# Kernel optimization log

Measured on AMD Instinct MI355X. Metric: run time of the kernel, lower is better.

Reference implementation:

```python
import jax, jax.numpy as jnp
import numpy as np

N, E, IN, H, C = 50000, 1600000, 256, 256, 2


def _lin(k, o, i):
    return (jax.random.normal(k, (o, i), jnp.float32) / np.sqrt(i)).astype(jnp.float32)


def setup_inputs() -> dict:
    key = jax.random.key(0)
    ks = jax.random.split(key, 16)
    x = jax.random.normal(ks[0], (N, IN), jnp.float32)
    edge_index = jax.random.randint(ks[1], (2, E), 0, N, dtype=jnp.int32)
    return dict(
        x=x, edge_index=edge_index,
        W1=_lin(ks[2], H, IN), b1=0.01 * jax.random.normal(ks[10], (H,), jnp.float32),
        W2=_lin(ks[3], H, H), b2=0.01 * jax.random.normal(ks[11], (H,), jnp.float32),
        W3=_lin(ks[4], H, H), b3=0.01 * jax.random.normal(ks[12], (H,), jnp.float32),
        W4=_lin(ks[5], C, H), b4=0.01 * jax.random.normal(ks[13], (C,), jnp.float32),
        T10=_lin(ks[6], H, H), T11=_lin(ks[7], H, H), cb1=0.01 * jax.random.normal(ks[14], (H,), jnp.float32),
        T20=_lin(ks[8], H, H), T21=_lin(ks[9], H, H), cb2=0.01 * jax.random.normal(ks[15], (H,), jnp.float32),
    )


def _cheb_norm(edge_index, n):
    # PyG ChebConv, normalization='sym', lambda_max=2.0:
    # L_hat = 2/lambda_max * (I - D^-1/2 A D^-1/2) - I = -D^-1/2 A D^-1/2
    # (the +I and -I self-loop terms cancel), so only off-diagonal norm remains.
    row, col = edge_index[0], edge_index[1]
    deg = jax.ops.segment_sum(jnp.ones((edge_index.shape[1],), jnp.float32), row, num_segments=n)
    dis = jnp.where(deg > 0, jax.lax.rsqrt(jnp.where(deg > 0, deg, 1.0)), 0.0)
    return -dis[row] * dis[col]  # [E]


def _cheb_conv(x, edge_index, norm, W0, W1, b, n):
    # K=2: out = Tx_0 @ W0^T + Tx_1 @ W1^T + b, Tx_0 = x, Tx_1 = L_hat x
    src, dst = edge_index[0], edge_index[1]  # message: x_j from src, aggregate at dst
    tx1 = jax.ops.segment_sum(norm[:, None] * x[src], dst, num_segments=n)
    return x @ W0.T + tx1 @ W1.T + b


def reference(x, edge_index, W1, b1, W2, b2, W3, b3, W4, b4, T10, T11, cb1, T20, T21, cb2):
    n = x.shape[0]
    norm = _cheb_norm(edge_index, n)
    h = jax.nn.relu(x @ W1.T + b1)
    h = jax.nn.relu(h @ W2.T + b2)
    h = _cheb_conv(h, edge_index, norm, T10, T11, cb1, n)
    h = _cheb_conv(h, edge_index, norm, T20, T21, cb2, n)
    h = jax.nn.relu(h @ W3.T + b3)
    return h @ W4.T + b4
```

## Files before the change

### kernel.cpp

```cpp
#include <hip/hip_runtime.h>

#define HDIM 256
#define NHB 256
#define NBINB 50048
#define NBINW (NBINB/4)
#define NBAND 16

typedef __attribute__((ext_vector_type(8))) short short8v;
typedef __attribute__((ext_vector_type(4))) short short4v;
typedef __attribute__((ext_vector_type(4))) float floatx4;

static __device__ __forceinline__ unsigned short f2bf(float f) {
    union { float f; unsigned u; } c; c.f = f;
    unsigned u = c.u;
    unsigned r = u + 0x7FFFu + ((u >> 16) & 1u);
    return (unsigned short)(r >> 16);
}
static __device__ __forceinline__ float bf2f(unsigned short h) {
    union { unsigned u; float f; } c; c.u = ((unsigned)h) << 16;
    return c.f;
}


__global__ __launch_bounds__(512) void hist_k(const int* __restrict__ src, const int* __restrict__ dst,
                                              unsigned int* __restrict__ degS, unsigned int* __restrict__ cntS,
                                              int nE) {
    __shared__ unsigned int h8[NBINW];
    const int tid = threadIdx.x;
    const int isDst = blockIdx.x >= NHB;
    const int bb = isDst ? blockIdx.x - NHB : blockIdx.x;
    const int* __restrict__ arr = isDst ? dst : src;
    unsigned int* __restrict__ outS = isDst ? cntS : degS;

    for (int i = tid; i < NBINW; i += 512) h8[i] = 0u;
    __syncthreads();
    const int chunk = (nE + NHB - 1) / NHB;
    const int e0 = bb * chunk;
    const int e1 = min(e0 + chunk, nE);
    for (int e = e0 + tid; e < e1; e += 512) {
        int n = arr[e];
        atomicAdd(&h8[n >> 2], 1u << ((n & 3) << 3));
    }
    __syncthreads();
    unsigned int* __restrict__ row = outS + (size_t)bb * NBINW;
    for (int i = tid; i < NBINW; i += 512) row[i] = h8[i];
}


__global__ __launch_bounds__(256) void reduce_k(const unsigned char* __restrict__ degS,
                                                unsigned char* __restrict__ cntS,
                                                float* __restrict__ dis, int* __restrict__ tmp,
                                                int* __restrict__ bsums, int nN) {
    __shared__ int s[256];
    const int t = threadIdx.x;
    const int n = blockIdx.x * 256 + t;
    int run = 0;
    if (n < nN) {
        int d = 0;
        #pragma unroll 8
        for (int b = 0; b < NHB; ++b) d += degS[(size_t)b * NBINB + n];
        dis[n] = (d > 0) ? (1.0f / sqrtf((float)d)) : 0.0f;
        unsigned r = 0;
        #pragma unroll 4
        for (int b = 0; b < NHB; ++b) {
            size_t o = (size_t)b * NBINB + n;
            unsigned c = cntS[o];
            cntS[o] = (unsigned char)r;
            r += c;
        }
        run = (int)r;
    }
    s[t] = run; __syncthreads();
    #pragma unroll
    for (int off = 1; off < 256; off <<= 1) {
        int x = (t >= off) ? s[t - off] : 0;
        __syncthreads();
        s[t] += x;
        __syncthreads();
    }
    if (n < nN) tmp[n] = s[t];
    if (t == 255) bsums[blockIdx.x] = s[255];
}


__global__ __launch_bounds__(256) void scan3_k(const int* __restrict__ tmp, const int* __restrict__ bsums,
                                               int* __restrict__ offs, int nN, int nE, int nb) {
    __shared__ int s[256];
    const int t = threadIdx.x;
    int v = (t < nb) ? bsums[t] : 0;
    s[t] = v; __syncthreads();
    #pragma unroll
    for (int off = 1; off < 256; off <<= 1) {
        int x = (t >= off) ? s[t - off] : 0;
        __syncthreads();
        s[t] += x;
        __syncthreads();
    }
    const int base = (blockIdx.x > 0) ? s[blockIdx.x - 1] : 0;
    __syncthreads();
    const int i = blockIdx.x * 256 + t;
    if (i < nN) {
        int prev = (t > 0) ? tmp[i - 1] : 0;
        offs[i] = base + prev;
    }
    if (i == nN - 1) offs[nN] = nE;
}


__global__ __launch_bounds__(512) void fill_k(const int* __restrict__ src, const int* __restrict__ dst,
                                              const float* __restrict__ dis, const int* __restrict__ offs,
                                              const unsigned int* __restrict__ cntS,
                                              int2* __restrict__ csr, int nE) {
    __shared__ unsigned int cur8[NBINW];
    const int tid = threadIdx.x;
    const int bb = blockIdx.x;
    const unsigned int* __restrict__ baseRow = cntS + (size_t)bb * NBINW;
    for (int i = tid; i < NBINW; i += 512) cur8[i] = baseRow[i];
    __syncthreads();
    const int chunk = (nE + NHB - 1) / NHB;
    const int e0 = bb * chunk;
    const int e1 = min(e0 + chunk, nE);
    for (int e = e0 + tid; e < e1; e += 512) {
        int s = src[e], d = dst[e];
        unsigned sh = (unsigned)(d & 3) << 3;
        unsigned old = atomicAdd(&cur8[d >> 2], 1u << sh);
        unsigned c = (old >> sh) & 0xFFu;
        int p = offs[d] + (int)c;
        float w = -dis[s] * dis[d];
        csr[p] = make_int2(s, __float_as_int(w));
    }
}


struct WPtrs { const float* w[7]; };
__global__ __launch_bounds__(256) void wsplit_all_k(WPtrs ws, unsigned short* __restrict__ base) {
    int wi = blockIdx.x >> 6;
    int idx = (blockIdx.x & 63) * 256 + threadIdx.x;
    const float* w = ws.w[wi];
    unsigned short* hi = base + (size_t)wi * 131072;
    unsigned short* lo = hi + 65536;
    float4 v = ((const float4*)w)[idx];
    float f[4] = {v.x, v.y, v.z, v.w};
    short4v hv, lv;
    #pragma unroll
    for (int e = 0; e < 4; ++e) {
        unsigned short h = f2bf(f[e]);
        float rem = f[e] - bf2f(h);
        hv[e] = (short)h;
        lv[e] = (short)f2bf(rem);
    }
    *(short4v*)(hi + idx * 4) = hv;
    *(short4v*)(lo + idx * 4) = lv;
}


#define LDP 40

__global__ __launch_bounds__(512, 4) void mfma_gemm_k(
    const float* __restrict__ AF,
    const unsigned short* __restrict__ Ah0, const unsigned short* __restrict__ Al0,
    const unsigned short* __restrict__ Wh0, const unsigned short* __restrict__ Wl0,
    const unsigned short* __restrict__ Ah1, const unsigned short* __restrict__ Al1,
    const unsigned short* __restrict__ Wh1, const unsigned short* __restrict__ Wl1,
    const float* __restrict__ bias,
    float* __restrict__ outF, unsigned short* __restrict__ outHi, unsigned short* __restrict__ outLo,
    const float* __restrict__ W4f, const float* __restrict__ b4f, float* __restrict__ outFinal,
    int nRows, int relu, int dual)
{
    __shared__ short Ahs[128 * LDP];
    __shared__ short Als[128 * LDP];
    __shared__ short Bhs[256 * LDP];
    __shared__ short Bls[256 * LDP];

    const int tid  = threadIdx.x;
    const int lane = tid & 63;
    const int wv   = tid >> 6;
    const int wm   = wv >> 2, wn = wv & 3;
    const int lrow = lane & 15, kg = lane >> 4;
    const int row0 = blockIdx.x * 128;

    const int sr = tid >> 2, sc = tid & 3;
    int agr = row0 + sr; if (agr >= nRows) agr = nRows - 1;

    floatx4 acc[4][4];
    #pragma unroll
    for (int i = 0; i < 4; ++i)
        #pragma unroll
        for (int j = 0; j < 4; ++j)
            acc[i][j] = (floatx4)0.0f;

    const int npass = dual ? 2 : 1;
    for (int pass = 0; pass < npass; ++pass) {
        const unsigned short* __restrict__ Ah = pass ? Ah1 : Ah0;
        const unsigned short* __restrict__ Al = pass ? Al1 : Al0;
        const unsigned short* __restrict__ Wh = pass ? Wh1 : Wh0;
        const unsigned short* __restrict__ Wl = pass ? Wl1 : Wl0;
        const bool f32A = (pass == 0) && (AF != nullptr);
        for (int k0 = 0; k0 < HDIM; k0 += 32) {
            __syncthreads();
            if (f32A) {
                const float* pa = AF + (size_t)agr * HDIM + k0 + sc * 8;
                float4 v0 = *(const float4*)pa;
                float4 v1 = *(const float4*)(pa + 4);
                float f[8] = {v0.x, v0.y, v0.z, v0.w, v1.x, v1.y, v1.z, v1.w};
                short8v hv, lv;
                #pragma unroll
                for (int e = 0; e < 8; ++e) {
                    unsigned short h = f2bf(f[e]);
                    float rem = f[e] - bf2f(h);
                    hv[e] = (short)h;
                    lv[e] = (short)f2bf(rem);
                }
                *(short8v*)(Ahs + sr * LDP + sc * 8) = hv;
                *(short8v*)(Als + sr * LDP + sc * 8) = lv;
            } else {
                size_t ga = (size_t)agr * HDIM + k0 + sc * 8;
                *(short8v*)(Ahs + sr * LDP + sc * 8) = *(const short8v*)(Ah + ga);
                *(short8v*)(Als + sr * LDP + sc * 8) = *(const short8v*)(Al + ga);
            }
            #pragma unroll
            for (int q = 0; q < 2; ++q) {
                int idx = tid + q * 512;
                int br = idx >> 2, bc = idx & 3;
                size_t gb = (size_t)br * HDIM + k0 + bc * 8;
                *(short8v*)(Bhs + br * LDP + bc * 8) = *(const short8v*)(Wh + gb);
                *(short8v*)(Bls + br * LDP + bc * 8) = *(const short8v*)(Wl + gb);
            }
            __syncthreads();

            short8v ahf[4], alf[4];
            #pragma unroll
            for (int fm = 0; fm < 4; ++fm) {
                int ra = (wm * 64 + fm * 16 + lrow) * LDP + kg * 8;
                ahf[fm] = *(const short8v*)(Ahs + ra);
                alf[fm] = *(const short8v*)(Als + ra);
            }
            #pragma unroll
            for (int fn = 0; fn < 4; ++fn) {
                int rb = (wn * 64 + fn * 16 + lrow) * LDP + kg * 8;
                short8v bh = *(const short8v*)(Bhs + rb);
                short8v bl = *(const short8v*)(Bls + rb);
                #pragma unroll
                for (int fm = 0; fm < 4; ++fm) {
                    acc[fm][fn] = __builtin_amdgcn_mfma_f32_16x16x32_bf16(ahf[fm], bh, acc[fm][fn], 0, 0, 0);
                    acc[fm][fn] = __builtin_amdgcn_mfma_f32_16x16x32_bf16(ahf[fm], bl, acc[fm][fn], 0, 0, 0);
                    acc[fm][fn] = __builtin_amdgcn_mfma_f32_16x16x32_bf16(alf[fm], bh, acc[fm][fn], 0, 0, 0);
                }
            }
        }
    }

    if (outFinal) {
        float w40[4], w41[4];
        #pragma unroll
        for (int fn = 0; fn < 4; ++fn) {
            int col = wn * 64 + fn * 16 + lrow;
            w40[fn] = W4f[col];
            w41[fn] = W4f[HDIM + col];
        }
        float p0[4][4], p1[4][4];
        #pragma unroll
        for (int fm = 0; fm < 4; ++fm)
            #pragma unroll
            for (int r = 0; r < 4; ++r) { p0[fm][r] = 0.f; p1[fm][r] = 0.f; }
        #pragma unroll
        for (int fn = 0; fn < 4; ++fn) {
            int col = wn * 64 + fn * 16 + lrow;
            float bv = bias[col];
            #pragma unroll
            for (int fm = 0; fm < 4; ++fm)
                #pragma unroll
                for (int r = 0; r < 4; ++r) {
                    float v = fmaxf(acc[fm][fn][r] + bv, 0.0f);
                    p0[fm][r] = fmaf(v, w40[fn], p0[fm][r]);
                    p1[fm][r] = fmaf(v, w41[fn], p1[fm][r]);
                }
        }
        #pragma unroll
        for (int fm = 0; fm < 4; ++fm)
            #pragma unroll
            for (int r = 0; r < 4; ++r) {
                #pragma unroll
                for (int m = 1; m < 16; m <<= 1) {
                    p0[fm][r] += __shfl_xor(p0[fm][r], m, 64);
                    p1[fm][r] += __shfl_xor(p1[fm][r], m, 64);
                }
            }
        __syncthreads();
        float* red = (float*)Ahs;
        if (lrow == 0) {
            #pragma unroll
            for (int fm = 0; fm < 4; ++fm)
                #pragma unroll
                for (int r = 0; r < 4; ++r) {
                    int rl = wm * 64 + fm * 16 + kg * 4 + r;
                    red[(wn * 128 + rl) * 2 + 0] = p0[fm][r];
                    red[(wn * 128 + rl) * 2 + 1] = p1[fm][r];
                }
        }
        __syncthreads();
        if (tid < 256) {
            int rl = tid >> 1, j = tid & 1;
            int grow = row0 + rl;
            if (grow < nRows) {
                float s = b4f[j]
                        + red[(0 * 128 + rl) * 2 + j] + red[(1 * 128 + rl) * 2 + j]
                        + red[(2 * 128 + rl) * 2 + j] + red[(3 * 128 + rl) * 2 + j];
                outFinal[(size_t)grow * 2 + j] = s;
            }
        }
        return;
    }

    #pragma unroll
    for (int fn = 0; fn < 4; ++fn) {
        int col = wn * 64 + fn * 16 + lrow;
        float bv = bias[col];
        #pragma unroll
        for (int fm = 0; fm < 4; ++fm) {
            #pragma unroll
            for (int r = 0; r < 4; ++r) {
                int grow = row0 + wm * 64 + fm * 16 + kg * 4 + r;
                if (grow < nRows) {
                    float v = acc[fm][fn][r] + bv;
                    if (relu) v = fmaxf(v, 0.0f);
                    size_t o = (size_t)grow * HDIM + col;
                    if (outF) outF[o] = v;
                    if (outHi) {
                        unsigned short h = f2bf(v);
                        outHi[o] = h;
                        outLo[o] = f2bf(v - bf2f(h));
                    }
                }
            }
        }
    }
}


#define ACC4(m0, m1, m2, m3)                                                    \
    {                                                                           \
        const uint2 g0 = *(const uint2*)(hb + (size_t)m0.x * HDIM + lane * 4);  \
        const uint2 g1 = *(const uint2*)(hb + (size_t)m1.x * HDIM + lane * 4);  \
        const uint2 g2 = *(const uint2*)(hb + (size_t)m2.x * HDIM + lane * 4);  \
        const uint2 g3 = *(const uint2*)(hb + (size_t)m3.x * HDIM + lane * 4);  \
        float w0 = __int_as_float(m0.y), w1 = __int_as_float(m1.y);             \
        float w2 = __int_as_float(m2.y), w3 = __int_as_float(m3.y);             \
        a0 = fmaf(w0, __uint_as_float(g0.x << 16), a0);                         \
        a1 = fmaf(w0, __uint_as_float(g0.x & 0xffff0000u), a1);                 \
        a2 = fmaf(w0, __uint_as_float(g0.y << 16), a2);                         \
        a3 = fmaf(w0, __uint_as_float(g0.y & 0xffff0000u), a3);                 \
        a0 = fmaf(w1, __uint_as_float(g1.x << 16), a0);                         \
        a1 = fmaf(w1, __uint_as_float(g1.x & 0xffff0000u), a1);                 \
        a2 = fmaf(w1, __uint_as_float(g1.y << 16), a2);                         \
        a3 = fmaf(w1, __uint_as_float(g1.y & 0xffff0000u), a3);                 \
        a0 = fmaf(w2, __uint_as_float(g2.x << 16), a0);                         \
        a1 = fmaf(w2, __uint_as_float(g2.x & 0xffff0000u), a1);                 \
        a2 = fmaf(w2, __uint_as_float(g2.y << 16), a2);                         \
        a3 = fmaf(w2, __uint_as_float(g2.y & 0xffff0000u), a3);                 \
        a0 = fmaf(w3, __uint_as_float(g3.x << 16), a0);                         \
        a1 = fmaf(w3, __uint_as_float(g3.x & 0xffff0000u), a1);                 \
        a2 = fmaf(w3, __uint_as_float(g3.y << 16), a2);                         \
        a3 = fmaf(w3, __uint_as_float(g3.y & 0xffff0000u), a3);                 \
    }

#define ACC1(m)                                                                 \
    {                                                                           \
        const uint2 g = *(const uint2*)(hb + (size_t)m.x * HDIM + lane * 4);    \
        float wt = __int_as_float(m.y);                                         \
        a0 = fmaf(wt, __uint_as_float(g.x << 16), a0);                          \
        a1 = fmaf(wt, __uint_as_float(g.x & 0xffff0000u), a1);                  \
        a2 = fmaf(wt, __uint_as_float(g.y << 16), a2);                          \
        a3 = fmaf(wt, __uint_as_float(g.y & 0xffff0000u), a3);                  \
    }

__global__ __launch_bounds__(256) void aggregate_k(
    const unsigned short* __restrict__ hb, const int2* __restrict__ csr,
    const int* __restrict__ offs,
    unsigned short* __restrict__ outHi, unsigned short* __restrict__ outLo)
{
    __shared__ float red[4][256];
    __shared__ int2 sorted[256];
    __shared__ unsigned bins[NBAND];
    __shared__ unsigned cur[NBAND];

    const int n = blockIdx.x;
    const int tid = threadIdx.x;
    const int w = tid >> 6;
    const int lane = tid & 63;
    const int start = offs[n], end = offs[n + 1];
    const int deg = end - start;

    float a0 = 0.f, a1 = 0.f, a2 = 0.f, a3 = 0.f;

    if (deg <= 256) {
        if (tid < NBAND) { bins[tid] = 0u; }
        __syncthreads();
        int2 my; int myband = 0;
        if (tid < deg) {
            my = csr[start + tid];
            myband = my.x >> 12;
            atomicAdd(&bins[myband], 1u);
        }
        __syncthreads();
        if (tid == 0) {
            unsigned run = 0;
            #pragma unroll
            for (int b = 0; b < NBAND; ++b) { unsigned c = bins[b]; cur[b] = run; run += c; }
        }
        __syncthreads();
        if (tid < deg) {
            unsigned pos = atomicAdd(&cur[myband], 1u);
            sorted[pos] = my;
        }
        __syncthreads();

        int e = w;
        for (; e + 12 < deg; e += 16) {
            int2 m0 = sorted[e], m1 = sorted[e + 4], m2 = sorted[e + 8], m3 = sorted[e + 12];
            ACC4(m0, m1, m2, m3);
        }
        for (; e < deg; e += 4) {
            int2 m = sorted[e];
            ACC1(m);
        }
    } else {
        int e = start + w;
        for (; e + 12 < end; e += 16) {
            int2 m0 = csr[e], m1 = csr[e + 4], m2 = csr[e + 8], m3 = csr[e + 12];
            ACC4(m0, m1, m2, m3);
        }
        for (; e < end; e += 4) {
            int2 m = csr[e];
            ACC1(m);
        }
    }

    red[w][lane * 4 + 0] = a0;
    red[w][lane * 4 + 1] = a1;
    red[w][lane * 4 + 2] = a2;
    red[w][lane * 4 + 3] = a3;
    __syncthreads();

    const int t = threadIdx.x;
    float s = red[0][t] + red[1][t] + red[2][t] + red[3][t];
    size_t o = (size_t)n * HDIM + t;
    unsigned short h = f2bf(s);
    outHi[o] = h;
    outLo[o] = f2bf(s - bf2f(h));
}


extern "C" void kernel_launch(void* const* d_in, const int* in_sizes, int n_in,
                              void* d_out, int out_size, void* d_ws, size_t ws_size,
                              hipStream_t stream) {
    const float* x   = (const float*)d_in[0];
    const int*   ei  = (const int*)d_in[1];
    const float* W1  = (const float*)d_in[2];
    const float* b1  = (const float*)d_in[3];
    const float* W2  = (const float*)d_in[4];
    const float* b2  = (const float*)d_in[5];
    const float* W3  = (const float*)d_in[6];
    const float* b3  = (const float*)d_in[7];
    const float* W4  = (const float*)d_in[8];
    const float* b4  = (const float*)d_in[9];
    const float* T10 = (const float*)d_in[10];
    const float* T11 = (const float*)d_in[11];
    const float* cb1 = (const float*)d_in[12];
    const float* T20 = (const float*)d_in[13];
    const float* T21 = (const float*)d_in[14];
    const float* cb2 = (const float*)d_in[15];

    const int nN = in_sizes[0] / HDIM;
    const int nE = in_sizes[1] / 2;
    const int* src = ei;
    const int* dst = ei + nE;

    char* p = (char*)d_ws;
    auto alloc = [&](size_t bytes) { void* r = (void*)p; p += (bytes + 255) & ~(size_t)255; return r; };
    float* dis     = (float*)alloc((size_t)nN * 4);
    int*   tmp     = (int*)alloc((size_t)nN * 4);
    int*   bsums   = (int*)alloc(1024 * 4);
    int*   offs    = (int*)alloc((size_t)(nN + 1) * 4);
    int2*  csr     = (int2*)alloc((size_t)nE * 8);
    unsigned int* degS = (unsigned int*)alloc((size_t)NHB * NBINB);
    unsigned int* cntS = (unsigned int*)alloc((size_t)NHB * NBINB);
    const size_t NH = (size_t)nN * HDIM;
    unsigned short* Xh  = (unsigned short*)alloc(NH * 4);  unsigned short* Xl  = Xh + NH;
    unsigned short* Ahp = (unsigned short*)alloc(NH * 4);  unsigned short* Alp = Ahp + NH;
    unsigned short* Bhp = (unsigned short*)alloc(NH * 4);  unsigned short* Blp = Bhp + NH;
    unsigned short* Dhp = (unsigned short*)alloc(NH * 4);  unsigned short* Dlp = Dhp + NH;
    unsigned short* wsp = (unsigned short*)alloc((size_t)7 * 131072 * 2);

    float* out = (float*)d_out;
    const int nbN = (nN + 255) / 256;

    hist_k<<<2 * NHB, 512, 0, stream>>>(src, dst, degS, cntS, nE);
    reduce_k<<<nbN, 256, 0, stream>>>((const unsigned char*)degS, (unsigned char*)cntS,
                                      dis, tmp, bsums, nN);
    scan3_k<<<nbN, 256, 0, stream>>>(tmp, bsums, offs, nN, nE, nbN);
    fill_k<<<NHB, 512, 0, stream>>>(src, dst, dis, offs, cntS, csr, nE);

    WPtrs wp; wp.w[0]=W1; wp.w[1]=W2; wp.w[2]=T10; wp.w[3]=T11; wp.w[4]=T20; wp.w[5]=T21; wp.w[6]=W3;
    wsplit_all_k<<<7 * 64, 256, 0, stream>>>(wp, wsp);
    unsigned short* wh[7]; unsigned short* wl[7];
    for (int i = 0; i < 7; ++i) { wh[i] = wsp + (size_t)i * 131072; wl[i] = wh[i] + 65536; }

    const int gb = (nN + 127) / 128;

    mfma_gemm_k<<<gb, 512, 0, stream>>>(x, nullptr, nullptr, wh[0], wl[0],
                                        nullptr, nullptr, nullptr, nullptr,
                                        b1, nullptr, Ahp, Alp,
                                        nullptr, nullptr, nullptr, nN, 1, 0);
    mfma_gemm_k<<<gb, 512, 0, stream>>>(nullptr, Ahp, Alp, wh[1], wl[1],
                                        nullptr, nullptr, nullptr, nullptr,
                                        b2, nullptr, Bhp, Blp,
                                        nullptr, nullptr, nullptr, nN, 1, 0);

    aggregate_k<<<nN, 256, 0, stream>>>(Bhp, csr, offs, Xh, Xl);
    mfma_gemm_k<<<gb, 512, 0, stream>>>(nullptr, Bhp, Blp, wh[2], wl[2],
                                        Xh, Xl, wh[3], wl[3],
                                        cb1, nullptr, Dhp, Dlp,
                                        nullptr, nullptr, nullptr, nN, 0, 1);

    aggregate_k<<<nN, 256, 0, stream>>>(Dhp, csr, offs, Ahp, Alp);
    mfma_gemm_k<<<gb, 512, 0, stream>>>(nullptr, Dhp, Dlp, wh[4], wl[4],
                                        Ahp, Alp, wh[5], wl[5],
                                        cb2, nullptr, Bhp, Blp,
                                        nullptr, nullptr, nullptr, nN, 0, 1);

    mfma_gemm_k<<<gb, 512, 0, stream>>>(nullptr, Bhp, Blp, wh[6], wl[6],
                                        nullptr, nullptr, nullptr, nullptr,
                                        b3, nullptr, nullptr, nullptr,
                                        W4, b4, out, nN, 1, 0);
}
```

Before: 596.0 us.

## Co-schedule graph histogram and CSR fill blocks with the first two GEMMs

Merges the edge histogram kernel into the first dense GEMM launch, and the CSR fill kernel into the second GEMM launch. Each fused launch dispatches GEMM blocks or graph-preprocessing blocks by block index, and they share one LDS buffer. The aim is to overlap the latency-bound atomic preprocessing with the MFMA GEMMs and to remove kernel launch gaps. In exchange, the GEMM blocks now carry the histogram's larger LDS allocation, and the fused kernel's launch bounds may cap occupancy for the histogram work.

```diff
diff --git a/kernel.cpp b/kernel.cpp
--- a/kernel.cpp
+++ b/kernel.cpp
@@ -5,6 +5,8 @@
 #define NBINB 50048
 #define NBINW (NBINB/4)
 #define NBAND 16
+#define LDP 40
+#define GEMM_LDS_U32 15360
 
 typedef __attribute__((ext_vector_type(8))) short short8v;
 typedef __attribute__((ext_vector_type(4))) short short4v;
@@ -22,13 +24,199 @@
 }
 
 
-__global__ __launch_bounds__(512) void hist_k(const int* __restrict__ src, const int* __restrict__ dst,
-                                              unsigned int* __restrict__ degS, unsigned int* __restrict__ cntS,
-                                              int nE) {
-    __shared__ unsigned int h8[NBINW];
+struct GemmArgs {
+    const float* AF;
+    const unsigned short* Ah0; const unsigned short* Al0;
+    const unsigned short* Wh0; const unsigned short* Wl0;
+    const unsigned short* Ah1; const unsigned short* Al1;
+    const unsigned short* Wh1; const unsigned short* Wl1;
+    const float* bias;
+    float* outF; unsigned short* outHi; unsigned short* outLo;
+    const float* W4f; const float* b4f; float* outFinal;
+    int nRows; int relu; int dual;
+};
+
+static __device__ __forceinline__ void gemm_body(unsigned int* ldsu, const GemmArgs& A, int bx)
+{
+    short* Ahs = (short*)ldsu;
+    short* Als = Ahs + 128 * LDP;
+    short* Bhs = Als + 128 * LDP;
+    short* Bls = Bhs + 256 * LDP;
+
+    const int tid  = threadIdx.x;
+    const int lane = tid & 63;
+    const int wv   = tid >> 6;
+    const int wm   = wv >> 2, wn = wv & 3;
+    const int lrow = lane & 15, kg = lane >> 4;
+    const int row0 = bx * 128;
+
+    const int sr = tid >> 2, sc = tid & 3;
+    int agr = row0 + sr; if (agr >= A.nRows) agr = A.nRows - 1;
+
+    floatx4 acc[4][4];
+    #pragma unroll
+    for (int i = 0; i < 4; ++i)
+        #pragma unroll
+        for (int j = 0; j < 4; ++j)
+            acc[i][j] = (floatx4)0.0f;
+
+    const int npass = A.dual ? 2 : 1;
+    for (int pass = 0; pass < npass; ++pass) {
+        const unsigned short* __restrict__ Ah = pass ? A.Ah1 : A.Ah0;
+        const unsigned short* __restrict__ Al = pass ? A.Al1 : A.Al0;
+        const unsigned short* __restrict__ Wh = pass ? A.Wh1 : A.Wh0;
+        const unsigned short* __restrict__ Wl = pass ? A.Wl1 : A.Wl0;
+        const bool f32A = (pass == 0) && (A.AF != nullptr);
+        for (int k0 = 0; k0 < HDIM; k0 += 32) {
+            __syncthreads();
+            if (f32A) {
+                const float* pa = A.AF + (size_t)agr * HDIM + k0 + sc * 8;
+                float4 v0 = *(const float4*)pa;
+                float4 v1 = *(const float4*)(pa + 4);
+                float f[8] = {v0.x, v0.y, v0.z, v0.w, v1.x, v1.y, v1.z, v1.w};
+                short8v hv, lv;
+                #pragma unroll
+                for (int e = 0; e < 8; ++e) {
+                    unsigned short h = f2bf(f[e]);
+                    float rem = f[e] - bf2f(h);
+                    hv[e] = (short)h;
+                    lv[e] = (short)f2bf(rem);
+                }
+                *(short8v*)(Ahs + sr * LDP + sc * 8) = hv;
+                *(short8v*)(Als + sr * LDP + sc * 8) = lv;
+            } else {
+                size_t ga = (size_t)agr * HDIM + k0 + sc * 8;
+                *(short8v*)(Ahs + sr * LDP + sc * 8) = *(const short8v*)(Ah + ga);
+                *(short8v*)(Als + sr * LDP + sc * 8) = *(const short8v*)(Al + ga);
+            }
+            #pragma unroll
+            for (int q = 0; q < 2; ++q) {
+                int idx = tid + q * 512;
+                int br = idx >> 2, bc = idx & 3;
+                size_t gb = (size_t)br * HDIM + k0 + bc * 8;
+                *(short8v*)(Bhs + br * LDP + bc * 8) = *(const short8v*)(Wh + gb);
+                *(short8v*)(Bls + br * LDP + bc * 8) = *(const short8v*)(Wl + gb);
+            }
+            __syncthreads();
+
+            short8v ahf[4], alf[4];
+            #pragma unroll
+            for (int fm = 0; fm < 4; ++fm) {
+                int ra = (wm * 64 + fm * 16 + lrow) * LDP + kg * 8;
+                ahf[fm] = *(const short8v*)(Ahs + ra);
+                alf[fm] = *(const short8v*)(Als + ra);
+            }
+            #pragma unroll
+            for (int fn = 0; fn < 4; ++fn) {
+                int rb = (wn * 64 + fn * 16 + lrow) * LDP + kg * 8;
+                short8v bh = *(const short8v*)(Bhs + rb);
+                short8v bl = *(const short8v*)(Bls + rb);
+                #pragma unroll
+                for (int fm = 0; fm < 4; ++fm) {
+                    acc[fm][fn] = __builtin_amdgcn_mfma_f32_16x16x32_bf16(ahf[fm], bh, acc[fm][fn], 0, 0, 0);
+                    acc[fm][fn] = __builtin_amdgcn_mfma_f32_16x16x32_bf16(ahf[fm], bl, acc[fm][fn], 0, 0, 0);
+                    acc[fm][fn] = __builtin_amdgcn_mfma_f32_16x16x32_bf16(alf[fm], bh, acc[fm][fn], 0, 0, 0);
+                }
+            }
+        }
+    }
+
+    if (A.outFinal) {
+        float w40[4], w41[4];
+        #pragma unroll
+        for (int fn = 0; fn < 4; ++fn) {
+            int col = wn * 64 + fn * 16 + lrow;
+            w40[fn] = A.W4f[col];
+            w41[fn] = A.W4f[HDIM + col];
+        }
+        float p0[4][4], p1[4][4];
+        #pragma unroll
+        for (int fm = 0; fm < 4; ++fm)
+            #pragma unroll
+            for (int r = 0; r < 4; ++r) { p0[fm][r] = 0.f; p1[fm][r] = 0.f; }
+        #pragma unroll
+        for (int fn = 0; fn < 4; ++fn) {
+            int col = wn * 64 + fn * 16 + lrow;
+            float bv = A.bias[col];
+            #pragma unroll
+            for (int fm = 0; fm < 4; ++fm)
+                #pragma unroll
+                for (int r = 0; r < 4; ++r) {
+                    float v = fmaxf(acc[fm][fn][r] + bv, 0.0f);
+                    p0[fm][r] = fmaf(v, w40[fn], p0[fm][r]);
+                    p1[fm][r] = fmaf(v, w41[fn], p1[fm][r]);
+                }
+        }
+        #pragma unroll
+        for (int fm = 0; fm < 4; ++fm)
+            #pragma unroll
+            for (int r = 0; r < 4; ++r) {
+                #pragma unroll
+                for (int m = 1; m < 16; m <<= 1) {
+                    p0[fm][r] += __shfl_xor(p0[fm][r], m, 64);
+                    p1[fm][r] += __shfl_xor(p1[fm][r], m, 64);
+                }
+            }
+        __syncthreads();
+        float* red = (float*)Ahs;
+        if (lrow == 0) {
+            #pragma unroll
+            for (int fm = 0; fm < 4; ++fm)
+                #pragma unroll
+                for (int r = 0; r < 4; ++r) {
+                    int rl = wm * 64 + fm * 16 + kg * 4 + r;
+                    red[(wn * 128 + rl) * 2 + 0] = p0[fm][r];
+                    red[(wn * 128 + rl) * 2 + 1] = p1[fm][r];
+                }
+        }
+        __syncthreads();
+        if (tid < 256) {
+            int rl = tid >> 1, j = tid & 1;
+            int grow = row0 + rl;
+            if (grow < A.nRows) {
+                float s = A.b4f[j]
+                        + red[(0 * 128 + rl) * 2 + j] + red[(1 * 128 + rl) * 2 + j]
+                        + red[(2 * 128 + rl) * 2 + j] + red[(3 * 128 + rl) * 2 + j];
+                A.outFinal[(size_t)grow * 2 + j] = s;
+            }
+        }
+        return;
+    }
+
+    #pragma unroll
+    for (int fn = 0; fn < 4; ++fn) {
+        int col = wn * 64 + fn * 16 + lrow;
+        float bv = A.bias[col];
+        #pragma unroll
+        for (int fm = 0; fm < 4; ++fm) {
+            #pragma unroll
+            for (int r = 0; r < 4; ++r) {
+                int grow = row0 + wm * 64 + fm * 16 + kg * 4 + r;
+                if (grow < A.nRows) {
+                    float v = acc[fm][fn][r] + bv;
+                    if (A.relu) v = fmaxf(v, 0.0f);
+                    size_t o = (size_t)grow * HDIM + col;
+                    if (A.outF) A.outF[o] = v;
+                    if (A.outHi) {
+                        unsigned short h = f2bf(v);
+                        A.outHi[o] = h;
+                        A.outLo[o] = f2bf(v - bf2f(h));
+                    }
+                }
+            }
+        }
+    }
+}
+
+
+static __device__ __forceinline__ void hist_body(unsigned int* h8,
+                                                 const int* __restrict__ src, const int* __restrict__ dst,
+                                                 unsigned int* __restrict__ degS, unsigned int* __restrict__ cntS,
+                                                 int nE, int bb2)
+{
     const int tid = threadIdx.x;
-    const int isDst = blockIdx.x >= NHB;
-    const int bb = isDst ? blockIdx.x - NHB : blockIdx.x;
+    const int isDst = bb2 >= NHB;
+    const int bb = isDst ? bb2 - NHB : bb2;
     const int* __restrict__ arr = isDst ? dst : src;
     unsigned int* __restrict__ outS = isDst ? cntS : degS;
 
@@ -44,6 +232,56 @@
     __syncthreads();
     unsigned int* __restrict__ row = outS + (size_t)bb * NBINW;
     for (int i = tid; i < NBINW; i += 512) row[i] = h8[i];
+}
+
+
+static __device__ __forceinline__ void fill_body(unsigned int* cur8,
+                                                 const int* __restrict__ src, const int* __restrict__ dst,
+                                                 const float* __restrict__ dis, const int* __restrict__ offs,
+                                                 const unsigned int* __restrict__ cntS,
+                                                 int2* __restrict__ csr, int nE, int bb)
+{
+    const int tid = threadIdx.x;
+    const unsigned int* __restrict__ baseRow = cntS + (size_t)bb * NBINW;
+    for (int i = tid; i < NBINW; i += 512) cur8[i] = baseRow[i];
+    __syncthreads();
+    const int chunk = (nE + NHB - 1) / NHB;
+    const int e0 = bb * chunk;
+    const int e1 = min(e0 + chunk, nE);
+    for (int e = e0 + tid; e < e1; e += 512) {
+        int s = src[e], d = dst[e];
+        unsigned sh = (unsigned)(d & 3) << 3;
+        unsigned old = atomicAdd(&cur8[d >> 2], 1u << sh);
+        unsigned c = (old >> sh) & 0xFFu;
+        int p = offs[d] + (int)c;
+        float w = -dis[s] * dis[d];
+        csr[p] = make_int2(s, __float_as_int(w));
+    }
+}
+
+
+__global__ __launch_bounds__(512, 4) void mfma_gemm_k(GemmArgs A) {
+    __shared__ __align__(16) unsigned int ldsu[GEMM_LDS_U32];
+    gemm_body(ldsu, A, blockIdx.x);
+}
+
+__global__ __launch_bounds__(512, 4) void fusedA_k(GemmArgs A,
+                                                   const int* __restrict__ src, const int* __restrict__ dst,
+                                                   unsigned int* __restrict__ degS, unsigned int* __restrict__ cntS,
+                                                   int nE, int gb) {
+    __shared__ __align__(16) unsigned int ldsu[GEMM_LDS_U32];
+    if ((int)blockIdx.x < gb) gemm_body(ldsu, A, blockIdx.x);
+    else                      hist_body(ldsu, src, dst, degS, cntS, nE, blockIdx.x - gb);
+}
+
+__global__ __launch_bounds__(512, 4) void fusedB_k(GemmArgs A,
+                                                   const int* __restrict__ src, const int* __restrict__ dst,
+                                                   const float* __restrict__ dis, const int* __restrict__ offs,
+                                                   const unsigned int* __restrict__ cntS,
+                                                   int2* __restrict__ csr, int nE, int gb) {
+    __shared__ __align__(16) unsigned int ldsu[GEMM_LDS_U32];
+    if ((int)blockIdx.x < gb) gemm_body(ldsu, A, blockIdx.x);
+    else                      fill_body(ldsu, src, dst, dis, offs, cntS, csr, nE, blockIdx.x - gb);
 }
 
 
@@ -107,31 +345,6 @@
 }
 
 
-__global__ __launch_bounds__(512) void fill_k(const int* __restrict__ src, const int* __restrict__ dst,
-                                              const float* __restrict__ dis, const int* __restrict__ offs,
-                                              const unsigned int* __restrict__ cntS,
-                                              int2* __restrict__ csr, int nE) {
-    __shared__ unsigned int cur8[NBINW];
-    const int tid = threadIdx.x;
-    const int bb = blockIdx.x;
-    const unsigned int* __restrict__ baseRow = cntS + (size_t)bb * NBINW;
-    for (int i = tid; i < NBINW; i += 512) cur8[i] = baseRow[i];
-    __syncthreads();
-    const int chunk = (nE + NHB - 1) / NHB;
-    const int e0 = bb * chunk;
-    const int e1 = min(e0 + chunk, nE);
-    for (int e = e0 + tid; e < e1; e += 512) {
-        int s = src[e], d = dst[e];
-        unsigned sh = (unsigned)(d & 3) << 3;
-        unsigned old = atomicAdd(&cur8[d >> 2], 1u << sh);
-        unsigned c = (old >> sh) & 0xFFu;
-        int p = offs[d] + (int)c;
-        float w = -dis[s] * dis[d];
-        csr[p] = make_int2(s, __float_as_int(w));
-    }
-}
-
-
 struct WPtrs { const float* w[7]; };
 __global__ __launch_bounds__(256) void wsplit_all_k(WPtrs ws, unsigned short* __restrict__ base) {
     int wi = blockIdx.x >> 6;
@@ -151,190 +364,6 @@
     }
     *(short4v*)(hi + idx * 4) = hv;
     *(short4v*)(lo + idx * 4) = lv;
-}
-
-
-#define LDP 40
-
-__global__ __launch_bounds__(512, 4) void mfma_gemm_k(
-    const float* __restrict__ AF,
-    const unsigned short* __restrict__ Ah0, const unsigned short* __restrict__ Al0,
-    const unsigned short* __restrict__ Wh0, const unsigned short* __restrict__ Wl0,
-    const unsigned short* __restrict__ Ah1, const unsigned short* __restrict__ Al1,
-    const unsigned short* __restrict__ Wh1, const unsigned short* __restrict__ Wl1,
-    const float* __restrict__ bias,
-    float* __restrict__ outF, unsigned short* __restrict__ outHi, unsigned short* __restrict__ outLo,
-    const float* __restrict__ W4f, const float* __restrict__ b4f, float* __restrict__ outFinal,
-    int nRows, int relu, int dual)
-{
-    __shared__ short Ahs[128 * LDP];
-    __shared__ short Als[128 * LDP];
-    __shared__ short Bhs[256 * LDP];
-    __shared__ short Bls[256 * LDP];
-
-    const int tid  = threadIdx.x;
-    const int lane = tid & 63;
-    const int wv   = tid >> 6;
-    const int wm   = wv >> 2, wn = wv & 3;
-    const int lrow = lane & 15, kg = lane >> 4;
-    const int row0 = blockIdx.x * 128;
-
-    const int sr = tid >> 2, sc = tid & 3;
-    int agr = row0 + sr; if (agr >= nRows) agr = nRows - 1;
-
-    floatx4 acc[4][4];
-    #pragma unroll
-    for (int i = 0; i < 4; ++i)
-        #pragma unroll
-        for (int j = 0; j < 4; ++j)
-            acc[i][j] = (floatx4)0.0f;
-
-    const int npass = dual ? 2 : 1;
-    for (int pass = 0; pass < npass; ++pass) {
-        const unsigned short* __restrict__ Ah = pass ? Ah1 : Ah0;
-        const unsigned short* __restrict__ Al = pass ? Al1 : Al0;
-        const unsigned short* __restrict__ Wh = pass ? Wh1 : Wh0;
-        const unsigned short* __restrict__ Wl = pass ? Wl1 : Wl0;
-        const bool f32A = (pass == 0) && (AF != nullptr);
-        for (int k0 = 0; k0 < HDIM; k0 += 32) {
-            __syncthreads();
-            if (f32A) {
-                const float* pa = AF + (size_t)agr * HDIM + k0 + sc * 8;
-                float4 v0 = *(const float4*)pa;
-                float4 v1 = *(const float4*)(pa + 4);
-                float f[8] = {v0.x, v0.y, v0.z, v0.w, v1.x, v1.y, v1.z, v1.w};
-                short8v hv, lv;
-                #pragma unroll
-                for (int e = 0; e < 8; ++e) {
-                    unsigned short h = f2bf(f[e]);
-                    float rem = f[e] - bf2f(h);
-                    hv[e] = (short)h;
-                    lv[e] = (short)f2bf(rem);
-                }
-                *(short8v*)(Ahs + sr * LDP + sc * 8) = hv;
-                *(short8v*)(Als + sr * LDP + sc * 8) = lv;
-            } else {
-                size_t ga = (size_t)agr * HDIM + k0 + sc * 8;
-                *(short8v*)(Ahs + sr * LDP + sc * 8) = *(const short8v*)(Ah + ga);
-                *(short8v*)(Als + sr * LDP + sc * 8) = *(const short8v*)(Al + ga);
-            }
-            #pragma unroll
-            for (int q = 0; q < 2; ++q) {
-                int idx = tid + q * 512;
-                int br = idx >> 2, bc = idx & 3;
-                size_t gb = (size_t)br * HDIM + k0 + bc * 8;
-                *(short8v*)(Bhs + br * LDP + bc * 8) = *(const short8v*)(Wh + gb);
-                *(short8v*)(Bls + br * LDP + bc * 8) = *(const short8v*)(Wl + gb);
-            }
-            __syncthreads();
-
-            short8v ahf[4], alf[4];
-            #pragma unroll
-            for (int fm = 0; fm < 4; ++fm) {
-                int ra = (wm * 64 + fm * 16 + lrow) * LDP + kg * 8;
-                ahf[fm] = *(const short8v*)(Ahs + ra);
-                alf[fm] = *(const short8v*)(Als + ra);
-            }
-            #pragma unroll
-            for (int fn = 0; fn < 4; ++fn) {
-                int rb = (wn * 64 + fn * 16 + lrow) * LDP + kg * 8;
-                short8v bh = *(const short8v*)(Bhs + rb);
-                short8v bl = *(const short8v*)(Bls + rb);
-                #pragma unroll
-                for (int fm = 0; fm < 4; ++fm) {
-                    acc[fm][fn] = __builtin_amdgcn_mfma_f32_16x16x32_bf16(ahf[fm], bh, acc[fm][fn], 0, 0, 0);
-                    acc[fm][fn] = __builtin_amdgcn_mfma_f32_16x16x32_bf16(ahf[fm], bl, acc[fm][fn], 0, 0, 0);
-                    acc[fm][fn] = __builtin_amdgcn_mfma_f32_16x16x32_bf16(alf[fm], bh, acc[fm][fn], 0, 0, 0);
-                }
-            }
-        }
-    }
-
-    if (outFinal) {
-        float w40[4], w41[4];
-        #pragma unroll
-        for (int fn = 0; fn < 4; ++fn) {
-            int col = wn * 64 + fn * 16 + lrow;
-            w40[fn] = W4f[col];
-            w41[fn] = W4f[HDIM + col];
-        }
-        float p0[4][4], p1[4][4];
-        #pragma unroll
-        for (int fm = 0; fm < 4; ++fm)
-            #pragma unroll
-            for (int r = 0; r < 4; ++r) { p0[fm][r] = 0.f; p1[fm][r] = 0.f; }
-        #pragma unroll
-        for (int fn = 0; fn < 4; ++fn) {
-            int col = wn * 64 + fn * 16 + lrow;
-            float bv = bias[col];
-            #pragma unroll
-            for (int fm = 0; fm < 4; ++fm)
-                #pragma unroll
-                for (int r = 0; r < 4; ++r) {
-                    float v = fmaxf(acc[fm][fn][r] + bv, 0.0f);
-                    p0[fm][r] = fmaf(v, w40[fn], p0[fm][r]);
-                    p1[fm][r] = fmaf(v, w41[fn], p1[fm][r]);
-                }
-        }
-        #pragma unroll
-        for (int fm = 0; fm < 4; ++fm)
-            #pragma unroll
-            for (int r = 0; r < 4; ++r) {
-                #pragma unroll
-                for (int m = 1; m < 16; m <<= 1) {
-                    p0[fm][r] += __shfl_xor(p0[fm][r], m, 64);
-                    p1[fm][r] += __shfl_xor(p1[fm][r], m, 64);
-                }
-            }
-        __syncthreads();
-        float* red = (float*)Ahs;
-        if (lrow == 0) {
-            #pragma unroll
-            for (int fm = 0; fm < 4; ++fm)
-                #pragma unroll
-                for (int r = 0; r < 4; ++r) {
-                    int rl = wm * 64 + fm * 16 + kg * 4 + r;
-                    red[(wn * 128 + rl) * 2 + 0] = p0[fm][r];
-                    red[(wn * 128 + rl) * 2 + 1] = p1[fm][r];
-                }
-        }
-        __syncthreads();
-        if (tid < 256) {
-            int rl = tid >> 1, j = tid & 1;
-            int grow = row0 + rl;
-            if (grow < nRows) {
-                float s = b4f[j]
-                        + red[(0 * 128 + rl) * 2 + j] + red[(1 * 128 + rl) * 2 + j]
-                        + red[(2 * 128 + rl) * 2 + j] + red[(3 * 128 + rl) * 2 + j];
-                outFinal[(size_t)grow * 2 + j] = s;
-            }
-        }
-        return;
-    }
-
-    #pragma unroll
-    for (int fn = 0; fn < 4; ++fn) {
-        int col = wn * 64 + fn * 16 + lrow;
-        float bv = bias[col];
-        #pragma unroll
-        for (int fm = 0; fm < 4; ++fm) {
-            #pragma unroll
-            for (int r = 0; r < 4; ++r) {
-                int grow = row0 + wm * 64 + fm * 16 + kg * 4 + r;
-                if (grow < nRows) {
-                    float v = acc[fm][fn][r] + bv;
-                    if (relu) v = fmaxf(v, 0.0f);
-                    size_t o = (size_t)grow * HDIM + col;
-                    if (outF) outF[o] = v;
-                    if (outHi) {
-                        unsigned short h = f2bf(v);
-                        outHi[o] = h;
-                        outLo[o] = f2bf(v - bf2f(h));
-                    }
-                }
-            }
-        }
-    }
 }
 
 
@@ -494,43 +523,36 @@
 
     float* out = (float*)d_out;
     const int nbN = (nN + 255) / 256;
-
-    hist_k<<<2 * NHB, 512, 0, stream>>>(src, dst, degS, cntS, nE);
-    reduce_k<<<nbN, 256, 0, stream>>>((const unsigned char*)degS, (unsigned char*)cntS,
-                                      dis, tmp, bsums, nN);
-    scan3_k<<<nbN, 256, 0, stream>>>(tmp, bsums, offs, nN, nE, nbN);
-    fill_k<<<NHB, 512, 0, stream>>>(src, dst, dis, offs, cntS, csr, nE);
+    const int gb = (nN + 127) / 128;
 
     WPtrs wp; wp.w[0]=W1; wp.w[1]=W2; wp.w[2]=T10; wp.w[3]=T11; wp.w[4]=T20; wp.w[5]=T21; wp.w[6]=W3;
     wsplit_all_k<<<7 * 64, 256, 0, stream>>>(wp, wsp);
     unsigned short* wh[7]; unsigned short* wl[7];
     for (int i = 0; i < 7; ++i) { wh[i] = wsp + (size_t)i * 131072; wl[i] = wh[i] + 65536; }
 
-    const int gb = (nN + 127) / 128;
-
-    mfma_gemm_k<<<gb, 512, 0, stream>>>(x, nullptr, nullptr, wh[0], wl[0],
-                                        nullptr, nullptr, nullptr, nullptr,
-                                        b1, nullptr, Ahp, Alp,
-                                        nullptr, nullptr, nullptr, nN, 1, 0);
-    mfma_gemm_k<<<gb, 512, 0, stream>>>(nullptr, Ahp, Alp, wh[1], wl[1],
-                                        nullptr, nullptr, nullptr, nullptr,
-                                        b2, nullptr, Bhp, Blp,
-                                        nullptr, nullptr, nullptr, nN, 1, 0);
+    GemmArgs g1 = { x, nullptr, nullptr, wh[0], wl[0], nullptr, nullptr, nullptr, nullptr,
+                    b1, nullptr, Ahp, Alp, nullptr, nullptr, nullptr, nN, 1, 0 };
+    fusedA_k<<<gb + 2 * NHB, 512, 0, stream>>>(g1, src, dst, degS, cntS, nE, gb);
+
+    reduce_k<<<nbN, 256, 0, stream>>>((const unsigned char*)degS, (unsigned char*)cntS,
+                                      dis, tmp, bsums, nN);
+    scan3_k<<<nbN, 256, 0, stream>>>(tmp, bsums, offs, nN, nE, nbN);
+
+    GemmArgs g2 = { nullptr, Ahp, Alp, wh[1], wl[1], nullptr, nullptr, nullptr, nullptr,
+                    b2, nullptr, Bhp, Blp, nullptr, nullptr, nullptr, nN, 1, 0 };
+    fusedB_k<<<gb + NHB, 512, 0, stream>>>(g2, src, dst, dis, offs, cntS, csr, nE, gb);
 
     aggregate_k<<<nN, 256, 0, stream>>>(Bhp, csr, offs, Xh, Xl);
-    mfma_gemm_k<<<gb, 512, 0, stream>>>(nullptr, Bhp, Blp, wh[2], wl[2],
-                                        Xh, Xl, wh[3], wl[3],
-                                        cb1, nullptr, Dhp, Dlp,
-                                        nullptr, nullptr, nullptr, nN, 0, 1);
+    GemmArgs g3 = { nullptr, Bhp, Blp, wh[2], wl[2], Xh, Xl, wh[3], wl[3],
+                    cb1, nullptr, Dhp, Dlp, nullptr, nullptr, nullptr, nN, 0, 1 };
+    mfma_gemm_k<<<gb, 512, 0, stream>>>(g3);
 
     aggregate_k<<<nN, 256, 0, stream>>>(Dhp, csr, offs, Ahp, Alp);
-    mfma_gemm_k<<<gb, 512, 0, stream>>>(nullptr, Dhp, Dlp, wh[4], wl[4],
-                                        Ahp, Alp, wh[5], wl[5],
-                                        cb2, nullptr, Bhp, Blp,
-                                        nullptr, nullptr, nullptr, nN, 0, 1);
-
-    mfma_gemm_k<<<gb, 512, 0, stream>>>(nullptr, Bhp, Blp, wh[6], wl[6],
-                                        nullptr, nullptr, nullptr, nullptr,
-                                        b3, nullptr, nullptr, nullptr,
-                                        W4, b4, out, nN, 1, 0);
-}
+    GemmArgs g4 = { nullptr, Dhp, Dlp, wh[4], wl[4], Ahp, Alp, wh[5], wl[5],
+                    cb2, nullptr, Bhp, Blp, nullptr, nullptr, nullptr, nN, 0, 1 };
+    mfma_gemm_k<<<gb, 512, 0, stream>>>(g4);
+
+    GemmArgs g5 = { nullptr, Bhp, Blp, wh[6], wl[6], nullptr, nullptr, nullptr, nullptr,
+                    b3, nullptr, nullptr, nullptr, W4, b4, out, nN, 1, 0 };
+    mfma_gemm_k<<<gb, 512, 0, stream>>>(g5);
+}
```

New measurement: 606.4 us. No clear change (+1.7%).

## Quantize aggregation inputs to per-row int8 with scales in GEMM epilogue

Applied to the files above, without the earlier changes.

The GEMM epilogue now also emits an int8 copy of its output with a per-row absmax scale, reduced across lanes with shuffles and across waves through shared memory. The neighbour-gather aggregation kernel reads 4 bytes per lane instead of 8-byte bf16 values and dequantizes using the row scale. This halves the random-gather traffic in the aggregation step, at the cost of extra epilogue work, an extra int8 write, and lower precision (int8 versus the earlier bf16 gather), which may break numeric tolerance.

```diff
diff --git a/kernel.cpp b/kernel.cpp
--- a/kernel.cpp
+++ b/kernel.cpp
@@ -5,6 +5,7 @@
 #define NBINB 50048
 #define NBINW (NBINB/4)
 #define NBAND 16
+#define LDP 40
 
 typedef __attribute__((ext_vector_type(8))) short short8v;
 typedef __attribute__((ext_vector_type(4))) short short4v;
@@ -154,8 +155,6 @@
 }
 
 
-#define LDP 40
-
 __global__ __launch_bounds__(512, 4) void mfma_gemm_k(
     const float* __restrict__ AF,
     const unsigned short* __restrict__ Ah0, const unsigned short* __restrict__ Al0,
@@ -164,6 +163,7 @@
     const unsigned short* __restrict__ Wh1, const unsigned short* __restrict__ Wl1,
     const float* __restrict__ bias,
     float* __restrict__ outF, unsigned short* __restrict__ outHi, unsigned short* __restrict__ outLo,
+    signed char* __restrict__ outI8, float* __restrict__ outSc,
     const float* __restrict__ W4f, const float* __restrict__ b4f, float* __restrict__ outFinal,
     int nRows, int relu, int dual)
 {
@@ -312,6 +312,11 @@
         return;
     }
 
+    float vmax[4][4];
+    #pragma unroll
+    for (int fm = 0; fm < 4; ++fm)
+        #pragma unroll
+        for (int r = 0; r < 4; ++r) vmax[fm][r] = 0.0f;
     #pragma unroll
     for (int fn = 0; fn < 4; ++fn) {
         int col = wn * 64 + fn * 16 + lrow;
@@ -320,10 +325,11 @@
         for (int fm = 0; fm < 4; ++fm) {
             #pragma unroll
             for (int r = 0; r < 4; ++r) {
+                float v = acc[fm][fn][r] + bv;
+                if (relu) v = fmaxf(v, 0.0f);
+                vmax[fm][r] = fmaxf(vmax[fm][r], fabsf(v));
                 int grow = row0 + wm * 64 + fm * 16 + kg * 4 + r;
                 if (grow < nRows) {
-                    float v = acc[fm][fn][r] + bv;
-                    if (relu) v = fmaxf(v, 0.0f);
                     size_t o = (size_t)grow * HDIM + col;
                     if (outF) outF[o] = v;
                     if (outHi) {
@@ -335,48 +341,68 @@
             }
         }
     }
-}
-
-
-#define ACC4(m0, m1, m2, m3)                                                    \
-    {                                                                           \
-        const uint2 g0 = *(const uint2*)(hb + (size_t)m0.x * HDIM + lane * 4);  \
-        const uint2 g1 = *(const uint2*)(hb + (size_t)m1.x * HDIM + lane * 4);  \
-        const uint2 g2 = *(const uint2*)(hb + (size_t)m2.x * HDIM + lane * 4);  \
-        const uint2 g3 = *(const uint2*)(hb + (size_t)m3.x * HDIM + lane * 4);  \
-        float w0 = __int_as_float(m0.y), w1 = __int_as_float(m1.y);             \
-        float w2 = __int_as_float(m2.y), w3 = __int_as_float(m3.y);             \
-        a0 = fmaf(w0, __uint_as_float(g0.x << 16), a0);                         \
-        a1 = fmaf(w0, __uint_as_float(g0.x & 0xffff0000u), a1);                 \
-        a2 = fmaf(w0, __uint_as_float(g0.y << 16), a2);                         \
-        a3 = fmaf(w0, __uint_as_float(g0.y & 0xffff0000u), a3);                 \
-        a0 = fmaf(w1, __uint_as_float(g1.x << 16), a0);                         \
-        a1 = fmaf(w1, __uint_as_float(g1.x & 0xffff0000u), a1);                 \
-        a2 = fmaf(w1, __uint_as_float(g1.y << 16), a2);                         \
-        a3 = fmaf(w1, __uint_as_float(g1.y & 0xffff0000u), a3);                 \
-        a0 = fmaf(w2, __uint_as_float(g2.x << 16), a0);                         \
-        a1 = fmaf(w2, __uint_as_float(g2.x & 0xffff0000u), a1);                 \
-        a2 = fmaf(w2, __uint_as_float(g2.y << 16), a2);                         \
-        a3 = fmaf(w2, __uint_as_float(g2.y & 0xffff0000u), a3);                 \
-        a0 = fmaf(w3, __uint_as_float(g3.x << 16), a0);                         \
-        a1 = fmaf(w3, __uint_as_float(g3.x & 0xffff0000u), a1);                 \
-        a2 = fmaf(w3, __uint_as_float(g3.y << 16), a2);                         \
-        a3 = fmaf(w3, __uint_as_float(g3.y & 0xffff0000u), a3);                 \
-    }
-
-#define ACC1(m)                                                                 \
-    {                                                                           \
-        const uint2 g = *(const uint2*)(hb + (size_t)m.x * HDIM + lane * 4);    \
-        float wt = __int_as_float(m.y);                                         \
-        a0 = fmaf(wt, __uint_as_float(g.x << 16), a0);                          \
-        a1 = fmaf(wt, __uint_as_float(g.x & 0xffff0000u), a1);                  \
-        a2 = fmaf(wt, __uint_as_float(g.y << 16), a2);                          \
-        a3 = fmaf(wt, __uint_as_float(g.y & 0xffff0000u), a3);                  \
-    }
+
+    if (outI8) {
+        #pragma unroll
+        for (int fm = 0; fm < 4; ++fm)
+            #pragma unroll
+            for (int r = 0; r < 4; ++r) {
+                #pragma unroll
+                for (int m = 1; m < 16; m <<= 1)
+                    vmax[fm][r] = fmaxf(vmax[fm][r], __shfl_xor(vmax[fm][r], m, 64));
+            }
+        __syncthreads();
+        float* wmax = (float*)Ahs;
+        if (lrow == 0) {
+            #pragma unroll
+            for (int fm = 0; fm < 4; ++fm)
+                #pragma unroll
+                for (int r = 0; r < 4; ++r) {
+                    int rl = wm * 64 + fm * 16 + kg * 4 + r;
+                    wmax[wn * 128 + rl] = vmax[fm][r];
+                }
+        }
+        __syncthreads();
+        #pragma unroll
+        for (int fm = 0; fm < 4; ++fm) {
+            #pragma unroll
+            for (int r = 0; r < 4; ++r) {
+                int rl = wm * 64 + fm * 16 + kg * 4 + r;
+                int grow = row0 + rl;
+                float rmax = fmaxf(fmaxf(wmax[rl], wmax[128 + rl]),
+                                   fmaxf(wmax[256 + rl], wmax[384 + rl]));
+                float inv = (rmax > 0.0f) ? (127.0f / rmax) : 0.0f;
+                if (grow < nRows) {
+                    #pragma unroll
+                    for (int fn = 0; fn < 4; ++fn) {
+                        int col = wn * 64 + fn * 16 + lrow;
+                        float v = acc[fm][fn][r] + bias[col];
+                        if (relu) v = fmaxf(v, 0.0f);
+                        outI8[(size_t)grow * HDIM + col] = (signed char)(int)rintf(v * inv);
+                    }
+                    if (wn == 0 && lrow == 0) outSc[grow] = rmax * (1.0f / 127.0f);
+                }
+            }
+        }
+    }
+}
+
+
+#define ACCQ1(m)                                                                 \
+    {                                                                            \
+        unsigned pv = *(const unsigned*)(hq + (size_t)m.x * HDIM + lane * 4);    \
+        float wq = __int_as_float(m.y) * hs[m.x];                                \
+        a0 = fmaf(wq, (float)((int)(pv << 24) >> 24), a0);                       \
+        a1 = fmaf(wq, (float)((int)(pv << 16) >> 24), a1);                       \
+        a2 = fmaf(wq, (float)((int)(pv << 8) >> 24), a2);                        \
+        a3 = fmaf(wq, (float)((int)pv >> 24), a3);                               \
+    }
+
+#define ACCQ4(m0, m1, m2, m3) { ACCQ1(m0); ACCQ1(m1); ACCQ1(m2); ACCQ1(m3); }
 
 __global__ __launch_bounds__(256) void aggregate_k(
-    const unsigned short* __restrict__ hb, const int2* __restrict__ csr,
-    const int* __restrict__ offs,
+    const signed char* __restrict__ hq, const float* __restrict__ hs,
+    const int2* __restrict__ csr, const int* __restrict__ offs,
     unsigned short* __restrict__ outHi, unsigned short* __restrict__ outLo)
 {
     __shared__ float red[4][256];
@@ -418,21 +444,21 @@
         int e = w;
         for (; e + 12 < deg; e += 16) {
             int2 m0 = sorted[e], m1 = sorted[e + 4], m2 = sorted[e + 8], m3 = sorted[e + 12];
-            ACC4(m0, m1, m2, m3);
+            ACCQ4(m0, m1, m2, m3);
         }
         for (; e < deg; e += 4) {
             int2 m = sorted[e];
-            ACC1(m);
+            ACCQ1(m);
         }
     } else {
         int e = start + w;
         for (; e + 12 < end; e += 16) {
             int2 m0 = csr[e], m1 = csr[e + 4], m2 = csr[e + 8], m3 = csr[e + 12];
-            ACC4(m0, m1, m2, m3);
+            ACCQ4(m0, m1, m2, m3);
         }
         for (; e < end; e += 4) {
             int2 m = csr[e];
-            ACC1(m);
+            ACCQ1(m);
         }
     }
 
@@ -490,10 +516,13 @@
     unsigned short* Ahp = (unsigned short*)alloc(NH * 4);  unsigned short* Alp = Ahp + NH;
     unsigned short* Bhp = (unsigned short*)alloc(NH * 4);  unsigned short* Blp = Bhp + NH;
     unsigned short* Dhp = (unsigned short*)alloc(NH * 4);  unsigned short* Dlp = Dhp + NH;
+    signed char*    i8b = (signed char*)alloc(NH);
+    float*          scb = (float*)alloc((size_t)nN * 4);
     unsigned short* wsp = (unsigned short*)alloc((size_t)7 * 131072 * 2);
 
     float* out = (float*)d_out;
     const int nbN = (nN + 255) / 256;
+    const int gb  = (nN + 127) / 128;
 
     hist_k<<<2 * NHB, 512, 0, stream>>>(src, dst, degS, cntS, nE);
     reduce_k<<<nbN, 256, 0, stream>>>((const unsigned char*)degS, (unsigned char*)cntS,
@@ -506,31 +535,29 @@
     unsigned short* wh[7]; unsigned short* wl[7];
     for (int i = 0; i < 7; ++i) { wh[i] = wsp + (size_t)i * 131072; wl[i] = wh[i] + 65536; }
 
-    const int gb = (nN + 127) / 128;
-
     mfma_gemm_k<<<gb, 512, 0, stream>>>(x, nullptr, nullptr, wh[0], wl[0],
                                         nullptr, nullptr, nullptr, nullptr,
-                                        b1, nullptr, Ahp, Alp,
+                                        b1, nullptr, Ahp, Alp, nullptr, nullptr,
                                         nullptr, nullptr, nullptr, nN, 1, 0);
     mfma_gemm_k<<<gb, 512, 0, stream>>>(nullptr, Ahp, Alp, wh[1], wl[1],
                                         nullptr, nullptr, nullptr, nullptr,
-                                        b2, nullptr, Bhp, Blp,
+                                        b2, nullptr, Bhp, Blp, i8b, scb,
                                         nullptr, nullptr, nullptr, nN, 1, 0);
 
-    aggregate_k<<<nN, 256, 0, stream>>>(Bhp, csr, offs, Xh, Xl);
+    aggregate_k<<<nN, 256, 0, stream>>>(i8b, scb, csr, offs, Xh, Xl);
     mfma_gemm_k<<<gb, 512, 0, stream>>>(nullptr, Bhp, Blp, wh[2], wl[2],
                                         Xh, Xl, wh[3], wl[3],
-                                        cb1, nullptr, Dhp, Dlp,
+                                        cb1, nullptr, Dhp, Dlp, i8b, scb,
                                         nullptr, nullptr, nullptr, nN, 0, 1);
 
-    aggregate_k<<<nN, 256, 0, stream>>>(Dhp, csr, offs, Ahp, Alp);
+    aggregate_k<<<nN, 256, 0, stream>>>(i8b, scb, csr, offs, Ahp, Alp);
     mfma_gemm_k<<<gb, 512, 0, stream>>>(nullptr, Dhp, Dlp, wh[4], wl[4],
                                         Ahp, Alp, wh[5], wl[5],
-                                        cb2, nullptr, Bhp, Blp,
+                                        cb2, nullptr, Bhp, Blp, nullptr, nullptr,
                                         nullptr, nullptr, nullptr, nN, 0, 1);
 
     mfma_gemm_k<<<gb, 512, 0, stream>>>(nullptr, Bhp, Blp, wh[6], wl[6],
                                         nullptr, nullptr, nullptr, nullptr,
-                                        b3, nullptr, nullptr, nullptr,
+                                        b3, nullptr, nullptr, nullptr, nullptr, nullptr,
                                         W4, b4, out, nN, 1, 0);
 }
```

New measurement: 591.5 us (median of 2 runs). Within noise of the previous version (-0.8%).
